# Kernel tuning notes

Measured on AMD Instinct MI355X. Metric: run time of the kernel, lower is better.

Reference implementation:

```python
import jax, jax.numpy as jnp
import numpy as np

H = 1024
V = 32000
L = 4096


def setup_inputs() -> dict:
    key = jax.random.key(0)
    ks = jax.random.split(key, 20)
    s = 1.0 / np.sqrt(H)
    d = {}
    d["input_token"] = jax.random.randint(ks[0], (1,), 0, V)
    d["hidden"] = jax.random.normal(ks[1], (1, 1, H), jnp.float32)
    d["encoder_hiddens"] = jax.random.normal(ks[2], (L, H), jnp.float32)
    # parameters
    d["emb"] = jax.random.normal(ks[3], (V, H), jnp.float32)
    d["wW"] = jax.random.uniform(ks[4], (H, H), jnp.float32, -s, s)
    d["wb"] = jax.random.uniform(ks[5], (H,), jnp.float32, -s, s)
    d["uW"] = jax.random.uniform(ks[6], (H, H), jnp.float32, -s, s)
    d["ub"] = jax.random.uniform(ks[7], (H,), jnp.float32, -s, s)
    d["vW"] = jax.random.uniform(ks[8], (1, H), jnp.float32, -s, s)
    d["cW"] = jax.random.uniform(ks[9], (H, 2 * H), jnp.float32, -s, s)
    d["cb"] = jax.random.uniform(ks[10], (H,), jnp.float32, -s, s)
    d["w_ih"] = jax.random.uniform(ks[11], (3 * H, H), jnp.float32, -s, s)
    d["b_ih"] = jax.random.uniform(ks[12], (3 * H,), jnp.float32, -s, s)
    d["w_hh"] = jax.random.uniform(ks[13], (3 * H, H), jnp.float32, -s, s)
    d["b_hh"] = jax.random.uniform(ks[14], (3 * H,), jnp.float32, -s, s)
    d["outW"] = jax.random.uniform(ks[15], (V, H), jnp.float32, -s, s)
    d["outb"] = jax.random.uniform(ks[16], (V,), jnp.float32, -s, s)
    return d


def reference(input_token, hidden, encoder_hiddens, emb, wW, wb, uW, ub, vW,
              cW, cb, w_ih, b_ih, w_hh, b_hh, outW, outb):
    # embedding lookup, dropout is identity (p=0 / eval)
    embedded = emb[input_token[0]]  # [H]
    # additive attention: w(hidden[0]) + u(enc) -> tanh -> v -> softmax
    h0 = hidden[0]  # [1, H] (first/only layer)
    scores = jnp.tanh(h0 @ wW.T + wb + encoder_hiddens @ uW.T + ub) @ vW[0]  # [L]
    attn_weights = jax.nn.softmax(scores, axis=-1)  # [L]
    context = attn_weights @ encoder_hiddens  # [H]
    # combine + relu
    x = jnp.concatenate([context, embedded])  # [2H]
    x = jax.nn.relu(x @ cW.T + cb)  # [H]
    # single GRU cell step (torch GRU gate order: r, z, n)
    hprev = hidden[0, 0]  # [H]
    gi = x @ w_ih.T + b_ih
    gh = hprev @ w_hh.T + b_hh
    ir, iz, inn = jnp.split(gi, 3)
    hr, hz, hn = jnp.split(gh, 3)
    r = jax.nn.sigmoid(ir + hr)
    z = jax.nn.sigmoid(iz + hz)
    n = jnp.tanh(inn + r * hn)
    hnew = (1.0 - z) * n + z * hprev  # [H]
    new_hidden = hnew.reshape(1, 1, H)
    # residual + output projection
    out = (context.reshape(1, 1, H) + new_hidden)
    logits = out @ outW.T + outb  # [1, 1, V]
    return logits, new_hidden, attn_weights
```

## Files before the change

### kernel.cpp

```cpp
#include <hip/hip_runtime.h>
#include <hip/hip_bf16.h>
#include <math.h>

#define H 1024
#define V 32000
#define L 4096

typedef __bf16 bf16x8 __attribute__((ext_vector_type(8)));
typedef float f32x4 __attribute__((ext_vector_type(4)));

__device__ __forceinline__ unsigned short f32_to_bf16(float f) {
    unsigned int u = __float_as_uint(f);
    unsigned int r = (u + 0x7fffu + ((u >> 16) & 1u)) >> 16;
    return (unsigned short)r;
}

__device__ __forceinline__ float dot4(float4 a, float4 b) {
    return a.x * b.x + a.y * b.y + a.z * b.z + a.w * b.w;
}

__device__ __forceinline__ float wave_reduce(float v) {
    for (int off = 32; off; off >>= 1) v += __shfl_xor(v, off);
    return v;
}

__global__ void prep_kernel(const float* __restrict__ enc,
                            const float* __restrict__ uW,
                            const float* __restrict__ emb,
                            const int* __restrict__ token,
                            unsigned short* __restrict__ enc_bf,
                            unsigned short* __restrict__ u_bf,
                            float* __restrict__ emb_vec) {
    int tid = blockIdx.x * blockDim.x + threadIdx.x;
    int stride = gridDim.x * blockDim.x;
    const int NE = L * H / 4;
    const int NU = H * H / 4;
    for (int i = tid; i < NE; i += stride) {
        float4 f = ((const float4*)enc)[i];
        ushort4 o;
        o.x = f32_to_bf16(f.x); o.y = f32_to_bf16(f.y);
        o.z = f32_to_bf16(f.z); o.w = f32_to_bf16(f.w);
        ((ushort4*)enc_bf)[i] = o;
    }
    for (int i = tid; i < NU; i += stride) {
        float4 f = ((const float4*)uW)[i];
        ushort4 o;
        o.x = f32_to_bf16(f.x); o.y = f32_to_bf16(f.y);
        o.z = f32_to_bf16(f.z); o.w = f32_to_bf16(f.w);
        ((ushort4*)u_bf)[i] = o;
    }
    int t0 = token[0];
    for (int i = tid; i < H; i += stride) emb_vec[i] = emb[(size_t)t0 * H + i];
}

__global__ void wh_kernel(const float* __restrict__ h0,
                          const float* __restrict__ wW,
                          const float* __restrict__ wb,
                          const float* __restrict__ ub,
                          float* __restrict__ wh) {
    int wave = (blockIdx.x * blockDim.x + threadIdx.x) >> 6;
    int lane = threadIdx.x & 63;
    if (wave >= H) return;
    const float4* row = (const float4*)(wW + (size_t)wave * H);
    const float4* hv = (const float4*)h0;
    float acc = 0.f;
    for (int i = 0; i < 4; i++) {
        int idx = i * 64 + lane;
        acc += dot4(row[idx], hv[idx]);
    }
    acc = wave_reduce(acc);
    if (lane == 0) wh[wave] = acc + wb[wave] + ub[wave];
}

#define APITCH 72
__global__ __launch_bounds__(256) void scores_kernel(
        const unsigned short* __restrict__ enc_bf,
        const unsigned short* __restrict__ u_bf,
        const float* __restrict__ wh,
        const float* __restrict__ vW,
        float* __restrict__ scores_part) {
    __shared__ unsigned short Als[64 * APITCH];
    __shared__ unsigned short Bls[256 * APITCH];
    int tid = threadIdx.x;
    int wave = tid >> 6, lane = tid & 63;
    int mrow = lane & 15, quad = lane >> 4;
    int r0 = blockIdx.x * 64;
    int jc0 = blockIdx.y * 256;

    f32x4 acc[16];
#pragma unroll
    for (int i = 0; i < 16; i++) acc[i] = (f32x4){0.f, 0.f, 0.f, 0.f};

    for (int k0 = 0; k0 < H; k0 += 64) {
#pragma unroll
        for (int c = 0; c < 2; c++) {
            int chunk = c * 256 + tid;
            int row = chunk >> 3, ko = (chunk & 7) * 8;
            uint4 v = *(const uint4*)(enc_bf + (size_t)(r0 + row) * H + k0 + ko);
            *(uint4*)(Als + row * APITCH + ko) = v;
        }
#pragma unroll
        for (int c = 0; c < 8; c++) {
            int chunk = c * 256 + tid;
            int j = chunk >> 3, ko = (chunk & 7) * 8;
            uint4 v = *(const uint4*)(u_bf + (size_t)(jc0 + j) * H + k0 + ko);
            *(uint4*)(Bls + j * APITCH + ko) = v;
        }
        __syncthreads();

        const unsigned short* abase = Als + (wave * 16 + mrow) * APITCH + quad * 8;
        bf16x8 a0 = *(const bf16x8*)(abase);
        bf16x8 a1 = *(const bf16x8*)(abase + 32);
#pragma unroll
        for (int jt = 0; jt < 16; jt++) {
            const unsigned short* bbase = Bls + (jt * 16 + mrow) * APITCH + quad * 8;
            bf16x8 b0 = *(const bf16x8*)(bbase);
            bf16x8 b1 = *(const bf16x8*)(bbase + 32);
            acc[jt] = __builtin_amdgcn_mfma_f32_16x16x32_bf16(a0, b0, acc[jt], 0, 0, 0);
            acc[jt] = __builtin_amdgcn_mfma_f32_16x16x32_bf16(a1, b1, acc[jt], 0, 0, 0);
        }
        __syncthreads();
    }

    float sacc[4] = {0.f, 0.f, 0.f, 0.f};
#pragma unroll
    for (int jt = 0; jt < 16; jt++) {
        int jcol = jc0 + jt * 16 + mrow;
        float vj = vW[jcol];
        float whv = wh[jcol];
#pragma unroll
        for (int r = 0; r < 4; r++) {
            sacc[r] += vj * tanhf(acc[jt][r] + whv);
        }
    }
#pragma unroll
    for (int r = 0; r < 4; r++) {
        float s = sacc[r];
        s += __shfl_xor(s, 1);
        s += __shfl_xor(s, 2);
        s += __shfl_xor(s, 4);
        s += __shfl_xor(s, 8);
        if (mrow == 0)
            scores_part[blockIdx.y * L + r0 + wave * 16 + quad * 4 + r] = s;
    }
}

__global__ __launch_bounds__(1024) void softmax_kernel(
        const float* __restrict__ scores_part,
        float* __restrict__ attn_ws,
        float* __restrict__ attn_out) {
    __shared__ float smax[16];
    __shared__ float ssum[16];
    int tid = threadIdx.x;
    int wid = tid >> 6, lane = tid & 63;
    float4 sv = ((const float4*)scores_part)[tid];
#pragma unroll
    for (int c = 1; c < 4; c++) {
        float4 p = ((const float4*)(scores_part + c * L))[tid];
        sv.x += p.x; sv.y += p.y; sv.z += p.z; sv.w += p.w;
    }
    float vmax = fmaxf(fmaxf(sv.x, sv.y), fmaxf(sv.z, sv.w));
    for (int off = 32; off; off >>= 1) vmax = fmaxf(vmax, __shfl_xor(vmax, off));
    if (lane == 0) smax[wid] = vmax;
    __syncthreads();
    if (tid == 0) {
        float m = smax[0];
        for (int i = 1; i < 16; i++) m = fmaxf(m, smax[i]);
        smax[0] = m;
    }
    __syncthreads();
    float gmax = smax[0];
    float e0 = expf(sv.x - gmax), e1 = expf(sv.y - gmax);
    float e2 = expf(sv.z - gmax), e3 = expf(sv.w - gmax);
    float s = e0 + e1 + e2 + e3;
    s = wave_reduce(s);
    if (lane == 0) ssum[wid] = s;
    __syncthreads();
    if (tid == 0) {
        float t = 0.f;
        for (int i = 0; i < 16; i++) t += ssum[i];
        ssum[0] = t;
    }
    __syncthreads();
    float inv = 1.0f / ssum[0];
    float4 o = make_float4(e0 * inv, e1 * inv, e2 * inv, e3 * inv);
    ((float4*)attn_ws)[tid] = o;
    ((float4*)attn_out)[tid] = o;
}

__global__ void context_kernel(const float* __restrict__ enc,
                               const float* __restrict__ attn,
                               float* __restrict__ context) {
    int col = blockIdx.x * 256 + threadIdx.x;
    int l0 = blockIdx.y * 32;
    float acc = 0.f;
    for (int l = l0; l < l0 + 32; l++) acc += attn[l] * enc[(size_t)l * H + col];
    atomicAdd(&context[col], acc);
}

__global__ void combine_kernel(const float* __restrict__ context,
                               const float* __restrict__ emb_vec,
                               const float* __restrict__ cW,
                               const float* __restrict__ cb,
                               float* __restrict__ xvec) {
    int wave = (blockIdx.x * blockDim.x + threadIdx.x) >> 6;
    int lane = threadIdx.x & 63;
    if (wave >= H) return;
    const float4* row = (const float4*)(cW + (size_t)wave * 2 * H);
    const float4* cv = (const float4*)context;
    const float4* ev = (const float4*)emb_vec;
    float acc = 0.f;
    for (int i = 0; i < 4; i++) {
        int idx = i * 64 + lane;
        acc += dot4(row[idx], cv[idx]);
        acc += dot4(row[256 + idx], ev[idx]);
    }
    acc = wave_reduce(acc);
    if (lane == 0) xvec[wave] = fmaxf(acc + cb[wave], 0.f);
}

__global__ void gru_kernel(const float* __restrict__ xvec,
                           const float* __restrict__ hprev,
                           const float* __restrict__ w_ih,
                           const float* __restrict__ b_ih,
                           const float* __restrict__ w_hh,
                           const float* __restrict__ b_hh,
                           const float* __restrict__ context,
                           float* __restrict__ hnew_out,
                           float* __restrict__ ovec) {
    int j = (blockIdx.x * blockDim.x + threadIdx.x) >> 6;
    int lane = threadIdx.x & 63;
    if (j >= H) return;
    const float4* xv = (const float4*)xvec;
    const float4* hv = (const float4*)hprev;
    float a0 = 0.f, a1 = 0.f, a2 = 0.f, a3 = 0.f, a4 = 0.f, a5 = 0.f;
    for (int i = 0; i < 4; i++) {
        int idx = i * 64 + lane;
        float4 x4 = xv[idx], h4 = hv[idx];
        a0 += dot4(((const float4*)(w_ih + (size_t)j * H))[idx], x4);
        a1 += dot4(((const float4*)(w_ih + (size_t)(H + j) * H))[idx], x4);
        a2 += dot4(((const float4*)(w_ih + (size_t)(2 * H + j) * H))[idx], x4);
        a3 += dot4(((const float4*)(w_hh + (size_t)j * H))[idx], h4);
        a4 += dot4(((const float4*)(w_hh + (size_t)(H + j) * H))[idx], h4);
        a5 += dot4(((const float4*)(w_hh + (size_t)(2 * H + j) * H))[idx], h4);
    }
    a0 = wave_reduce(a0); a1 = wave_reduce(a1); a2 = wave_reduce(a2);
    a3 = wave_reduce(a3); a4 = wave_reduce(a4); a5 = wave_reduce(a5);
    if (lane == 0) {
        float ir = a0 + b_ih[j], iz = a1 + b_ih[H + j], inn = a2 + b_ih[2 * H + j];
        float hr = a3 + b_hh[j], hz = a4 + b_hh[H + j], hn = a5 + b_hh[2 * H + j];
        float r = 1.f / (1.f + expf(-(ir + hr)));
        float z = 1.f / (1.f + expf(-(iz + hz)));
        float n = tanhf(inn + r * hn);
        float hp = hprev[j];
        float hval = (1.f - z) * n + z * hp;
        hnew_out[j] = hval;
        ovec[j] = context[j] + hval;
    }
}

__global__ void logits_kernel(const float* __restrict__ ovec,
                              const float* __restrict__ outW,
                              const float* __restrict__ outb,
                              float* __restrict__ out) {
    int i = (blockIdx.x * blockDim.x + threadIdx.x) >> 6;
    int lane = threadIdx.x & 63;
    if (i >= V) return;
    const float4* row = (const float4*)(outW + (size_t)i * H);
    const float4* ov = (const float4*)ovec;
    float acc = 0.f;
    for (int t = 0; t < 4; t++) {
        int idx = t * 64 + lane;
        acc += dot4(row[idx], ov[idx]);
    }
    acc = wave_reduce(acc);
    if (lane == 0) out[i] = acc + outb[i];
}

extern "C" void kernel_launch(void* const* d_in, const int* in_sizes, int n_in,
                              void* d_out, int out_size, void* d_ws, size_t ws_size,
                              hipStream_t stream) {
    const int* token = (const int*)d_in[0];
    const float* hidden = (const float*)d_in[1];
    const float* enc = (const float*)d_in[2];
    const float* emb = (const float*)d_in[3];
    const float* wW = (const float*)d_in[4];
    const float* wb = (const float*)d_in[5];
    const float* uW = (const float*)d_in[6];
    const float* ub = (const float*)d_in[7];
    const float* vW = (const float*)d_in[8];
    const float* cW = (const float*)d_in[9];
    const float* cb = (const float*)d_in[10];
    const float* w_ih = (const float*)d_in[11];
    const float* b_ih = (const float*)d_in[12];
    const float* w_hh = (const float*)d_in[13];
    const float* b_hh = (const float*)d_in[14];
    const float* outW = (const float*)d_in[15];
    const float* outb = (const float*)d_in[16];
    float* out = (float*)d_out;

    char* ws = (char*)d_ws;
    unsigned short* enc_bf = (unsigned short*)ws;
    unsigned short* u_bf = (unsigned short*)(ws + (size_t)L * H * 2);
    float* whv = (float*)(ws + (size_t)L * H * 2 + (size_t)H * H * 2);
    float* emb_vec = whv + H;
    float* scores_part = emb_vec + H;
    float* attn = scores_part + 4 * L;
    float* context = attn + L;
    float* xvec = context + H;
    float* ovec = xvec + H;

    hipMemsetAsync(context, 0, H * sizeof(float), stream);
    prep_kernel<<<1024, 256, 0, stream>>>(enc, uW, emb, token, enc_bf, u_bf, emb_vec);
    wh_kernel<<<256, 256, 0, stream>>>(hidden, wW, wb, ub, whv);
    scores_kernel<<<dim3(64, 4), 256, 0, stream>>>(enc_bf, u_bf, whv, vW, scores_part);
    softmax_kernel<<<1, 1024, 0, stream>>>(scores_part, attn, out + V + H);
    context_kernel<<<dim3(4, 128), 256, 0, stream>>>(enc, attn, context);
    combine_kernel<<<256, 256, 0, stream>>>(context, emb_vec, cW, cb, xvec);
    gru_kernel<<<256, 256, 0, stream>>>(xvec, hidden, w_ih, b_ih, w_hh, b_hh,
                                        context, out + V, ovec);
    logits_kernel<<<8000, 256, 0, stream>>>(ovec, outW, outb, out);
}
```

Baseline: 355.9 us.

## Fuse prep and wh kernels, shrink score tiles, fold memset, two rows per logits wave

```diff
diff --git a/kernel.cpp b/kernel.cpp
--- a/kernel.cpp
+++ b/kernel.cpp
@@ -24,52 +24,54 @@
     return v;
 }
 
-__global__ void prep_kernel(const float* __restrict__ enc,
-                            const float* __restrict__ uW,
-                            const float* __restrict__ emb,
-                            const int* __restrict__ token,
-                            unsigned short* __restrict__ enc_bf,
-                            unsigned short* __restrict__ u_bf,
-                            float* __restrict__ emb_vec) {
-    int tid = blockIdx.x * blockDim.x + threadIdx.x;
-    int stride = gridDim.x * blockDim.x;
-    const int NE = L * H / 4;
-    const int NU = H * H / 4;
-    for (int i = tid; i < NE; i += stride) {
-        float4 f = ((const float4*)enc)[i];
-        ushort4 o;
-        o.x = f32_to_bf16(f.x); o.y = f32_to_bf16(f.y);
-        o.z = f32_to_bf16(f.z); o.w = f32_to_bf16(f.w);
-        ((ushort4*)enc_bf)[i] = o;
-    }
-    for (int i = tid; i < NU; i += stride) {
-        float4 f = ((const float4*)uW)[i];
-        ushort4 o;
-        o.x = f32_to_bf16(f.x); o.y = f32_to_bf16(f.y);
-        o.z = f32_to_bf16(f.z); o.w = f32_to_bf16(f.w);
-        ((ushort4*)u_bf)[i] = o;
-    }
-    int t0 = token[0];
-    for (int i = tid; i < H; i += stride) emb_vec[i] = emb[(size_t)t0 * H + i];
-}
-
-__global__ void wh_kernel(const float* __restrict__ h0,
-                          const float* __restrict__ wW,
-                          const float* __restrict__ wb,
-                          const float* __restrict__ ub,
-                          float* __restrict__ wh) {
-    int wave = (blockIdx.x * blockDim.x + threadIdx.x) >> 6;
-    int lane = threadIdx.x & 63;
-    if (wave >= H) return;
-    const float4* row = (const float4*)(wW + (size_t)wave * H);
-    const float4* hv = (const float4*)h0;
-    float acc = 0.f;
-    for (int i = 0; i < 4; i++) {
-        int idx = i * 64 + lane;
-        acc += dot4(row[idx], hv[idx]);
-    }
-    acc = wave_reduce(acc);
-    if (lane == 0) wh[wave] = acc + wb[wave] + ub[wave];
+__global__ __launch_bounds__(256) void prep_wh_kernel(
+        const float* __restrict__ enc,
+        const float* __restrict__ uW,
+        const float* __restrict__ emb,
+        const int* __restrict__ token,
+        const float* __restrict__ h0,
+        const float* __restrict__ wW,
+        const float* __restrict__ wb,
+        const float* __restrict__ ub,
+        unsigned short* __restrict__ enc_bf,
+        unsigned short* __restrict__ u_bf,
+        float* __restrict__ emb_vec,
+        float* __restrict__ wh) {
+    if (blockIdx.x < 1024) {
+        int tid = blockIdx.x * 256 + threadIdx.x;
+        const int stride = 1024 * 256;
+        const int NE = L * H / 4;
+        const int NU = H * H / 4;
+        for (int i = tid; i < NE; i += stride) {
+            float4 f = ((const float4*)enc)[i];
+            ushort4 o;
+            o.x = f32_to_bf16(f.x); o.y = f32_to_bf16(f.y);
+            o.z = f32_to_bf16(f.z); o.w = f32_to_bf16(f.w);
+            ((ushort4*)enc_bf)[i] = o;
+        }
+        for (int i = tid; i < NU; i += stride) {
+            float4 f = ((const float4*)uW)[i];
+            ushort4 o;
+            o.x = f32_to_bf16(f.x); o.y = f32_to_bf16(f.y);
+            o.z = f32_to_bf16(f.z); o.w = f32_to_bf16(f.w);
+            ((ushort4*)u_bf)[i] = o;
+        }
+        int t0 = token[0];
+        for (int i = tid; i < H; i += stride) emb_vec[i] = emb[(size_t)t0 * H + i];
+    } else {
+        int wave = ((blockIdx.x - 1024) * 256 + threadIdx.x) >> 6;
+        int lane = threadIdx.x & 63;
+        const float4* row = (const float4*)(wW + (size_t)wave * H);
+        const float4* hv = (const float4*)h0;
+        float acc = 0.f;
+#pragma unroll
+        for (int i = 0; i < 4; i++) {
+            int idx = i * 64 + lane;
+            acc += dot4(row[idx], hv[idx]);
+        }
+        acc = wave_reduce(acc);
+        if (lane == 0) wh[wave] = acc + wb[wave] + ub[wave];
+    }
 }
 
 #define APITCH 72
@@ -79,41 +81,41 @@
         const float* __restrict__ wh,
         const float* __restrict__ vW,
         float* __restrict__ scores_part) {
-    __shared__ unsigned short Als[64 * APITCH];
-    __shared__ unsigned short Bls[256 * APITCH];
+    __shared__ unsigned short Als[32 * APITCH];
+    __shared__ unsigned short Bls[128 * APITCH];
     int tid = threadIdx.x;
     int wave = tid >> 6, lane = tid & 63;
+    int wm = wave >> 1, wn = wave & 1;
     int mrow = lane & 15, quad = lane >> 4;
-    int r0 = blockIdx.x * 64;
-    int jc0 = blockIdx.y * 256;
-
-    f32x4 acc[16];
-#pragma unroll
-    for (int i = 0; i < 16; i++) acc[i] = (f32x4){0.f, 0.f, 0.f, 0.f};
+    int r0b = blockIdx.x * 32;
+    int jc0b = blockIdx.y * 128;
+
+    f32x4 acc[4];
+#pragma unroll
+    for (int i = 0; i < 4; i++) acc[i] = (f32x4){0.f, 0.f, 0.f, 0.f};
 
     for (int k0 = 0; k0 < H; k0 += 64) {
-#pragma unroll
-        for (int c = 0; c < 2; c++) {
-            int chunk = c * 256 + tid;
-            int row = chunk >> 3, ko = (chunk & 7) * 8;
-            uint4 v = *(const uint4*)(enc_bf + (size_t)(r0 + row) * H + k0 + ko);
+        {
+            int row = tid >> 3, ko = (tid & 7) * 8;
+            uint4 v = *(const uint4*)(enc_bf + (size_t)(r0b + row) * H + k0 + ko);
             *(uint4*)(Als + row * APITCH + ko) = v;
         }
 #pragma unroll
-        for (int c = 0; c < 8; c++) {
+        for (int c = 0; c < 4; c++) {
             int chunk = c * 256 + tid;
             int j = chunk >> 3, ko = (chunk & 7) * 8;
-            uint4 v = *(const uint4*)(u_bf + (size_t)(jc0 + j) * H + k0 + ko);
+            uint4 v = *(const uint4*)(u_bf + (size_t)(jc0b + j) * H + k0 + ko);
             *(uint4*)(Bls + j * APITCH + ko) = v;
         }
         __syncthreads();
 
-        const unsigned short* abase = Als + (wave * 16 + mrow) * APITCH + quad * 8;
+        const unsigned short* abase = Als + (wm * 16 + mrow) * APITCH + quad * 8;
         bf16x8 a0 = *(const bf16x8*)(abase);
         bf16x8 a1 = *(const bf16x8*)(abase + 32);
 #pragma unroll
-        for (int jt = 0; jt < 16; jt++) {
-            const unsigned short* bbase = Bls + (jt * 16 + mrow) * APITCH + quad * 8;
+        for (int jt = 0; jt < 4; jt++) {
+            const unsigned short* bbase =
+                Bls + (wn * 64 + jt * 16 + mrow) * APITCH + quad * 8;
             bf16x8 b0 = *(const bf16x8*)(bbase);
             bf16x8 b1 = *(const bf16x8*)(bbase + 32);
             acc[jt] = __builtin_amdgcn_mfma_f32_16x16x32_bf16(a0, b0, acc[jt], 0, 0, 0);
@@ -124,8 +126,8 @@
 
     float sacc[4] = {0.f, 0.f, 0.f, 0.f};
 #pragma unroll
-    for (int jt = 0; jt < 16; jt++) {
-        int jcol = jc0 + jt * 16 + mrow;
+    for (int jt = 0; jt < 4; jt++) {
+        int jcol = jc0b + wn * 64 + jt * 16 + mrow;
         float vj = vW[jcol];
         float whv = wh[jcol];
 #pragma unroll
@@ -141,21 +143,23 @@
         s += __shfl_xor(s, 4);
         s += __shfl_xor(s, 8);
         if (mrow == 0)
-            scores_part[blockIdx.y * L + r0 + wave * 16 + quad * 4 + r] = s;
+            scores_part[(blockIdx.y * 2 + wn) * L + r0b + wm * 16 + quad * 4 + r] = s;
     }
 }
 
 __global__ __launch_bounds__(1024) void softmax_kernel(
         const float* __restrict__ scores_part,
         float* __restrict__ attn_ws,
-        float* __restrict__ attn_out) {
+        float* __restrict__ attn_out,
+        float* __restrict__ context) {
     __shared__ float smax[16];
     __shared__ float ssum[16];
     int tid = threadIdx.x;
     int wid = tid >> 6, lane = tid & 63;
+    context[tid] = 0.f;
     float4 sv = ((const float4*)scores_part)[tid];
 #pragma unroll
-    for (int c = 1; c < 4; c++) {
+    for (int c = 1; c < 16; c++) {
         float4 p = ((const float4*)(scores_part + c * L))[tid];
         sv.x += p.x; sv.y += p.y; sv.z += p.z; sv.w += p.w;
     }
@@ -210,6 +214,7 @@
     const float4* cv = (const float4*)context;
     const float4* ev = (const float4*)emb_vec;
     float acc = 0.f;
+#pragma unroll
     for (int i = 0; i < 4; i++) {
         int idx = i * 64 + lane;
         acc += dot4(row[idx], cv[idx]);
@@ -234,6 +239,7 @@
     const float4* xv = (const float4*)xvec;
     const float4* hv = (const float4*)hprev;
     float a0 = 0.f, a1 = 0.f, a2 = 0.f, a3 = 0.f, a4 = 0.f, a5 = 0.f;
+#pragma unroll
     for (int i = 0; i < 4; i++) {
         int idx = i * 64 + lane;
         float4 x4 = xv[idx], h4 = hv[idx];
@@ -259,22 +265,32 @@
     }
 }
 
-__global__ void logits_kernel(const float* __restrict__ ovec,
-                              const float* __restrict__ outW,
-                              const float* __restrict__ outb,
-                              float* __restrict__ out) {
-    int i = (blockIdx.x * blockDim.x + threadIdx.x) >> 6;
+__global__ __launch_bounds__(256) void logits_kernel(
+        const float* __restrict__ ovec,
+        const float* __restrict__ outW,
+        const float* __restrict__ outb,
+        float* __restrict__ out) {
+    int wave = (blockIdx.x * blockDim.x + threadIdx.x) >> 6;
     int lane = threadIdx.x & 63;
-    if (i >= V) return;
-    const float4* row = (const float4*)(outW + (size_t)i * H);
+    int i0 = wave * 2;
+    if (i0 >= V) return;
+    const float4* row0 = (const float4*)(outW + (size_t)i0 * H);
+    const float4* row1 = (const float4*)(outW + (size_t)(i0 + 1) * H);
     const float4* ov = (const float4*)ovec;
-    float acc = 0.f;
+    float acc0 = 0.f, acc1 = 0.f;
+#pragma unroll
     for (int t = 0; t < 4; t++) {
         int idx = t * 64 + lane;
-        acc += dot4(row[idx], ov[idx]);
-    }
-    acc = wave_reduce(acc);
-    if (lane == 0) out[i] = acc + outb[i];
+        float4 o4 = ov[idx];
+        acc0 += dot4(row0[idx], o4);
+        acc1 += dot4(row1[idx], o4);
+    }
+    acc0 = wave_reduce(acc0);
+    acc1 = wave_reduce(acc1);
+    if (lane == 0) {
+        out[i0] = acc0 + outb[i0];
+        out[i0 + 1] = acc1 + outb[i0 + 1];
+    }
 }
 
 extern "C" void kernel_launch(void* const* d_in, const int* in_sizes, int n_in,
@@ -305,19 +321,18 @@
     float* whv = (float*)(ws + (size_t)L * H * 2 + (size_t)H * H * 2);
     float* emb_vec = whv + H;
     float* scores_part = emb_vec + H;
-    float* attn = scores_part + 4 * L;
+    float* attn = scores_part + 16 * L;
     float* context = attn + L;
     float* xvec = context + H;
     float* ovec = xvec + H;
 
-    hipMemsetAsync(context, 0, H * sizeof(float), stream);
-    prep_kernel<<<1024, 256, 0, stream>>>(enc, uW, emb, token, enc_bf, u_bf, emb_vec);
-    wh_kernel<<<256, 256, 0, stream>>>(hidden, wW, wb, ub, whv);
-    scores_kernel<<<dim3(64, 4), 256, 0, stream>>>(enc_bf, u_bf, whv, vW, scores_part);
-    softmax_kernel<<<1, 1024, 0, stream>>>(scores_part, attn, out + V + H);
+    prep_wh_kernel<<<1280, 256, 0, stream>>>(enc, uW, emb, token, hidden, wW, wb, ub,
+                                             enc_bf, u_bf, emb_vec, whv);
+    scores_kernel<<<dim3(128, 8), 256, 0, stream>>>(enc_bf, u_bf, whv, vW, scores_part);
+    softmax_kernel<<<1, 1024, 0, stream>>>(scores_part, attn, out + V + H, context);
     context_kernel<<<dim3(4, 128), 256, 0, stream>>>(enc, attn, context);
     combine_kernel<<<256, 256, 0, stream>>>(context, emb_vec, cW, cb, xvec);
     gru_kernel<<<256, 256, 0, stream>>>(xvec, hidden, w_ih, b_ih, w_hh, b_hh,
                                         context, out + V, ovec);
-    logits_kernel<<<8000, 256, 0, stream>>>(ovec, outW, outb, out);
-}
+    logits_kernel<<<4000, 256, 0, stream>>>(ovec, outW, outb, out);
+}
```

New measurement: 355.8 us. No clear change (-0.0%).
